# Kernel tuning notes

Measured on AMD Instinct MI355X. Metric: run time of the kernel, lower is better.

The kernel has to match this reference:

```python
import jax, jax.numpy as jnp
import numpy as np

B, IN, H = 8192, 512, 512


def _binarize(w):
    # sign() forward with straight-through gradient (ebnn Binarize)
    return w + jax.lax.stop_gradient(jnp.sign(w) - w)


def setup_inputs() -> dict:
    key = jax.random.key(0)
    ks = jax.random.split(key, 7)
    stdv = 1.0 / np.sqrt(H)
    return {
        "x": jax.random.normal(ks[0], (B, IN), jnp.float32),
        "hx": jax.random.normal(ks[1], (B, H), jnp.float32),
        "cx": jax.random.normal(ks[2], (B, H), jnp.float32),
        "W_ih": jax.random.uniform(ks[3], (4 * H, IN), jnp.float32, -stdv, stdv),
        "W_hh": jax.random.uniform(ks[4], (4 * H, H), jnp.float32, -stdv, stdv),
        "bias_ih": jax.random.uniform(ks[5], (4 * H,), jnp.float32, -stdv, stdv),
        "bias_hh": jax.random.uniform(ks[6], (4 * H,), jnp.float32, -stdv, stdv),
    }


def reference(x, hx, cx, W_ih, W_hh, bias_ih, bias_hh):
    # gates: [B, 4H] = x @ sign(W_ih)^T + b_ih + hx @ sign(W_hh)^T + b_hh
    gates = (jnp.einsum("bi,gi->bg", x, _binarize(W_ih)) + bias_ih
             + jnp.einsum("bh,gh->bg", hx, _binarize(W_hh)) + bias_hh)
    ingate, forgetgate, cellgate, outgate = jnp.split(gates, 4, axis=1)
    cy = jax.nn.sigmoid(forgetgate) * cx + jax.nn.sigmoid(ingate) * jnp.tanh(cellgate)
    hy = jax.nn.sigmoid(outgate) * jnp.tanh(cy)
    return (hy, cy)
```

## Files before the change

kernel.cpp:

```cpp
#include <hip/hip_runtime.h>
#include <hip/hip_bf16.h>
#include <stdint.h>


typedef __attribute__((ext_vector_type(4))) int int4x;
typedef __attribute__((ext_vector_type(4))) float float4x;

#define B_DIM 8192
#define H_DIM 512

__device__ __forceinline__ float bf2f(uint16_t u) {
  return __uint_as_float(((uint32_t)u) << 16);
}
__device__ __forceinline__ uint16_t f2bf(float f) {
  uint32_t u = __float_as_uint(f);
  return (uint16_t)((u + 0x7FFFu + ((u >> 16) & 1u)) >> 16);
}
__device__ __forceinline__ float sigm(float x) { return 1.0f / (1.0f + __expf(-x)); }
__device__ __forceinline__ float tanh_f(float x) { return 2.0f / (1.0f + __expf(-2.0f * x)) - 1.0f; }

__device__ __forceinline__ int detect_f32(const void* x) {
  const int l = threadIdx.x & 63;
  uint32_t wrd = ((const uint32_t*)x)[l];
  uint32_t e0 = (wrd >> 7) & 0xFFu, e1 = (wrd >> 23) & 0xFFu;
  return __ballot(e0 > 0x85u || e1 > 0x85u) != 0ull;
}

__device__ __forceinline__ void quant4(const float* v, uint32_t* hi4, uint32_t* lo4) {
  uint32_t h = 0, lo = 0;
#pragma unroll
  for (int j = 0; j < 4; ++j) {
    float c = fminf(fmaxf(v[j], -8.0f), 8.0f);
    int xf = __float2int_rn(c * 4096.0f);
    xf = xf > 32639 ? 32639 : xf;
    xf = xf < -32768 ? -32768 : xf;
    const int lb = (xf << 24) >> 24;
    const int hb = (xf - lb) >> 8;
    lo |= ((uint32_t)lb & 0xFFu) << (8 * j);
    h |= ((uint32_t)hb & 0xFFu) << (8 * j);
  }
  *hi4 = h;
  *lo4 = lo;
}

__device__ __forceinline__ void gload16(const void* g, void* l) {
  __builtin_amdgcn_global_load_lds(
      (const __attribute__((address_space(1))) unsigned int*)g,
      (__attribute__((address_space(3))) unsigned int*)l, 16, 0, 0);
}

__global__ __launch_bounds__(256) void prep_kernel(
    const void* __restrict__ x, const void* __restrict__ hx,
    const void* __restrict__ w_ih, const void* __restrict__ w_hh,
    int8_t* __restrict__ Xhi, int8_t* __restrict__ Xlo, int8_t* __restrict__ Bp) {
  __shared__ alignas(16) char lsc[33280];
  const int isF32 = detect_f32(x);
  const int t = threadIdx.x;
  const int w = t >> 6, l = t & 63;
  const int isX = blockIdx.x < 512;
  const int grp = isX ? blockIdx.x : (blockIdx.x - 512);

#pragma unroll
  for (int rr = 0; rr < 4; ++rr) {
    const int r = w * 4 + rr;
    long rowbase;
    if (isX) rowbase = (long)(grp * 16 + r) * 512;
    else     rowbase = (long)((grp & 3) * 512 + (grp >> 2) * 16 + r) * 512;
#pragma unroll
    for (int src = 0; src < 2; ++src) {
      const void* sp_ = isX ? (src ? hx : x) : (src ? w_hh : w_ih);
#pragma unroll
      for (int q = 0; q < 2; ++q) {
        const int k = src * 512 + q * 256 + l * 4;
        float v[4];
        if (isF32) {
          float4x f = *(const float4x*)((const float*)sp_ + rowbase + q * 256 + l * 4);
          v[0] = f[0]; v[1] = f[1]; v[2] = f[2]; v[3] = f[3];
        } else {
          const uint16_t* s = (const uint16_t*)sp_ + rowbase + q * 256 + l * 4;
#pragma unroll
          for (int j = 0; j < 4; ++j) v[j] = bf2f(s[j]);
        }
        if (isX) {
          uint32_t h4, lo4;
          quant4(v, &h4, &lo4);
          *(uint32_t*)(lsc + r * 1040 + k) = h4;
          *(uint32_t*)(lsc + 16640 + r * 1040 + k) = lo4;
        } else {
          uint32_t s4 = 0;
#pragma unroll
          for (int j = 0; j < 4; ++j) {
            const int sv = v[j] > 0.f ? 1 : (v[j] < 0.f ? -1 : 0);
            s4 |= ((uint32_t)sv & 0xFFu) << (8 * j);
          }
          *(uint32_t*)(lsc + r * 1040 + k) = s4;
        }
      }
    }
  }
  __syncthreads();
  const int kt = t >> 4, quad = (t >> 2) & 3, rb = (t & 3) * 4;
  const int loff = kt * 64 + quad * 16;
  if (isX) {
    int4x h[4], lo[4];
#pragma unroll
    for (int i = 0; i < 4; ++i) {
      h[i] = *(const int4x*)(lsc + (rb + i) * 1040 + loff);
      lo[i] = *(const int4x*)(lsc + 16640 + (rb + i) * 1040 + loff);
    }
    int4x* dh = (int4x*)(Xhi + (long)grp * 16384 + t * 64);
    int4x* dl = (int4x*)(Xlo + (long)grp * 16384 + t * 64);
#pragma unroll
    for (int i = 0; i < 4; ++i) { dh[i] = h[i]; dl[i] = lo[i]; }
  } else {
    int4x s[4];
#pragma unroll
    for (int i = 0; i < 4; ++i)
      s[i] = *(const int4x*)(lsc + (rb + i) * 1040 + loff);
    int4x* db = (int4x*)(Bp + (long)grp * 16384 + t * 64);
#pragma unroll
    for (int i = 0; i < 4; ++i) db[i] = s[i];
  }
}

__global__ __launch_bounds__(256, 2) void blstm_gemm_kernel(
    const int8_t* __restrict__ Xhi, const int8_t* __restrict__ Xlo,
    const int8_t* __restrict__ Bp, const void* __restrict__ b_ih,
    const void* __restrict__ b_hh, const void* __restrict__ cx,
    const void* __restrict__ xdet, void* __restrict__ out) {
  __shared__ alignas(16) char lds[73728];
  const int tid = threadIdx.x;
  const int l = tid & 63, w = tid >> 6;
  const int lrow = l & 15, lq = l >> 4;
  const int wy = w >> 1, wx = w & 1;
  const int isF32 = detect_f32(xdet);
  const int bid = blockIdx.x;
  const int idx = bid >> 3;
  const int by = (bid & 7) * 8 + (idx >> 4);
  const int bx = idx & 15;

  const int8_t* csrc[6];
  int cdst[6];
#pragma unroll
  for (int i = 0; i < 6; ++i) {
    const int c = w * 6 + i;
    if (c < 8) {
      csrc[i] = Xhi + (((long)(by * 8 + c)) << 14) + l * 16;
      cdst[i] = c * 1024;
    } else if (c < 16) {
      csrc[i] = Xlo + (((long)(by * 8 + (c - 8))) << 14) + l * 16;
      cdst[i] = 8192 + (c - 8) * 1024;
    } else {
      csrc[i] = Bp + (((long)(bx * 8 + (c - 16))) << 14) + l * 16;
      cdst[i] = 16384 + (c - 16) * 1024;
    }
  }

  int4x acch[4][4], accl[4][4];
#pragma unroll
  for (int mt = 0; mt < 4; ++mt)
#pragma unroll
    for (int g = 0; g < 4; ++g) {
      acch[mt][g] = (int4x){0, 0, 0, 0};
      accl[mt][g] = (int4x){0, 0, 0, 0};
    }

#pragma unroll
  for (int i = 0; i < 6; ++i) gload16(csrc[i], lds + cdst[i]);
#pragma unroll
  for (int i = 0; i < 6; ++i) gload16(csrc[i] + 1024, lds + 24576 + cdst[i]);
  asm volatile("s_waitcnt vmcnt(6)\n\ts_barrier" ::: "memory");

#pragma unroll
  for (int ks = 0; ks < 16; ++ks) {
    const int cb = (ks % 3) * 24576;
    if (ks < 14) {
      const int nb = ((ks + 2) % 3) * 24576;
#pragma unroll
      for (int i = 0; i < 6; ++i)
        gload16(csrc[i] + (long)(ks + 2) * 1024, lds + nb + cdst[i]);
    }
    int4x ah[4], al[4], b[4];
#pragma unroll
    for (int mt = 0; mt < 4; ++mt) {
      ah[mt] = *(const int4x*)(lds + cb + (wy * 4 + mt) * 1024 + l * 16);
      al[mt] = *(const int4x*)(lds + cb + 8192 + (wy * 4 + mt) * 1024 + l * 16);
    }
#pragma unroll
    for (int g = 0; g < 4; ++g)
      b[g] = *(const int4x*)(lds + cb + 16384 + (wx * 4 + g) * 1024 + l * 16);
    __builtin_amdgcn_s_setprio(1);
#pragma unroll
    for (int mt = 0; mt < 4; ++mt)
#pragma unroll
      for (int g = 0; g < 4; ++g) {
        acch[mt][g] = __builtin_amdgcn_mfma_i32_16x16x64_i8(ah[mt], b[g], acch[mt][g], 0, 0, 0);
        accl[mt][g] = __builtin_amdgcn_mfma_i32_16x16x64_i8(al[mt], b[g], accl[mt][g], 0, 0, 0);
      }
    __builtin_amdgcn_s_setprio(0);
    if (ks < 14)
      asm volatile("s_waitcnt vmcnt(6)\n\ts_waitcnt lgkmcnt(0)\n\ts_barrier" ::: "memory");
    else if (ks == 14)
      asm volatile("s_waitcnt vmcnt(0)\n\ts_waitcnt lgkmcnt(0)\n\ts_barrier" ::: "memory");
  }

  const long CYo = (long)B_DIM * H_DIM;
  const int c = bx * 32 + wx * 16 + lrow;
  float biasv[4];
#pragma unroll
  for (int g = 0; g < 4; ++g) {
    if (isF32)
      biasv[g] = ((const float*)b_ih)[g * 512 + c] + ((const float*)b_hh)[g * 512 + c];
    else
      biasv[g] = bf2f(((const uint16_t*)b_ih)[g * 512 + c]) + bf2f(((const uint16_t*)b_hh)[g * 512 + c]);
  }
  float* outF = (float*)out;
  uint16_t* outB = (uint16_t*)out;
#pragma unroll
  for (int mt = 0; mt < 4; ++mt) {
#pragma unroll
    for (int r = 0; r < 4; ++r) {
      const int row = by * 128 + wy * 64 + mt * 16 + lq * 4 + r;
      const long cidx = (long)row * H_DIM + c;
      float vg[4];
#pragma unroll
      for (int g = 0; g < 4; ++g)
        vg[g] = fmaf((float)acch[mt][g][r], 0.0625f,
                     fmaf((float)accl[mt][g][r], 2.44140625e-4f, biasv[g]));
      const float cxv = isF32 ? ((const float*)cx)[cidx] : bf2f(((const uint16_t*)cx)[cidx]);
      const float ig = sigm(vg[0]), fg = sigm(vg[1]), og = sigm(vg[3]);
      const float cg = tanh_f(vg[2]);
      const float cy = fg * cxv + ig * cg;
      const float hy = og * tanh_f(cy);
      if (isF32) {
        outF[cidx] = hy;
        outF[CYo + cidx] = cy;
      } else {
        outB[cidx] = f2bf(hy);
        outB[CYo + cidx] = f2bf(cy);
      }
    }
  }
}

extern "C" void kernel_launch(void* const* d_in, const int* in_sizes, int n_in,
                              void* d_out, int out_size, void* d_ws, size_t ws_size,
                              hipStream_t stream) {
  const void* x = d_in[0];
  const void* hx = d_in[1];
  const void* cx = d_in[2];
  const void* W_ih = d_in[3];
  const void* W_hh = d_in[4];
  const void* b_ih = d_in[5];
  const void* b_hh = d_in[6];
  char* ws = (char*)d_ws;
  int8_t* Xhi = (int8_t*)ws;
  int8_t* Xlo = (int8_t*)(ws + 8388608);
  int8_t* Bp = (int8_t*)(ws + 16777216);

  prep_kernel<<<640, 256, 0, stream>>>(x, hx, W_ih, W_hh, Xhi, Xlo, Bp);
  blstm_gemm_kernel<<<1024, 256, 0, stream>>>(Xhi, Xlo, Bp, b_ih, b_hh, cx, x, d_out);
}
```

Baseline: 151.9 us.

## Double-buffer LDS and register fragments to fit three blocks per CU

Shrinks the LDS staging ring from three buffers to two and raises launch bounds to three blocks per CU. It adds a register double-buffer of MFMA operand fragments: the next k-step's fragments are read from LDS while the current step's MFMAs run. The aim is higher occupancy and hiding LDS read latency. In exchange, each step now waits for all global loads to drain (vmcnt(0)) before its barrier, so prefetch distance shrinks, and register pressure rises under a tighter VGPR budget, which risks spills.

```diff
diff --git a/kernel.cpp b/kernel.cpp
--- a/kernel.cpp
+++ b/kernel.cpp
@@ -123,12 +123,12 @@
   }
 }
 
-__global__ __launch_bounds__(256, 2) void blstm_gemm_kernel(
+__global__ __launch_bounds__(256, 3) void blstm_gemm_kernel(
     const int8_t* __restrict__ Xhi, const int8_t* __restrict__ Xlo,
     const int8_t* __restrict__ Bp, const void* __restrict__ b_ih,
     const void* __restrict__ b_hh, const void* __restrict__ cx,
     const void* __restrict__ xdet, void* __restrict__ out) {
-  __shared__ alignas(16) char lds[73728];
+  __shared__ alignas(16) char lds[49152];
   const int tid = threadIdx.x;
   const int l = tid & 63, w = tid >> 6;
   const int lrow = l & 15, lq = l >> 4;
@@ -165,43 +165,55 @@
       accl[mt][g] = (int4x){0, 0, 0, 0};
     }
 
+  int4x fr0[12], fr1[12];
+
 #pragma unroll
   for (int i = 0; i < 6; ++i) gload16(csrc[i], lds + cdst[i]);
 #pragma unroll
   for (int i = 0; i < 6; ++i) gload16(csrc[i] + 1024, lds + 24576 + cdst[i]);
   asm volatile("s_waitcnt vmcnt(6)\n\ts_barrier" ::: "memory");
+#pragma unroll
+  for (int mt = 0; mt < 4; ++mt) {
+    fr0[mt] = *(const int4x*)(lds + (wy * 4 + mt) * 1024 + l * 16);
+    fr0[4 + mt] = *(const int4x*)(lds + 8192 + (wy * 4 + mt) * 1024 + l * 16);
+  }
+#pragma unroll
+  for (int g = 0; g < 4; ++g)
+    fr0[8 + g] = *(const int4x*)(lds + 16384 + (wx * 4 + g) * 1024 + l * 16);
 
 #pragma unroll
   for (int ks = 0; ks < 16; ++ks) {
-    const int cb = (ks % 3) * 24576;
+    const int cur = ks & 1;
+    int4x* const frc = cur ? fr1 : fr0;
+    int4x* const frn = cur ? fr0 : fr1;
+    if (ks < 15) {
+      asm volatile("s_waitcnt vmcnt(0)\n\ts_waitcnt lgkmcnt(0)\n\ts_barrier" ::: "memory");
+    }
     if (ks < 14) {
-      const int nb = ((ks + 2) % 3) * 24576;
 #pragma unroll
       for (int i = 0; i < 6; ++i)
-        gload16(csrc[i] + (long)(ks + 2) * 1024, lds + nb + cdst[i]);
-    }
-    int4x ah[4], al[4], b[4];
-#pragma unroll
-    for (int mt = 0; mt < 4; ++mt) {
-      ah[mt] = *(const int4x*)(lds + cb + (wy * 4 + mt) * 1024 + l * 16);
-      al[mt] = *(const int4x*)(lds + cb + 8192 + (wy * 4 + mt) * 1024 + l * 16);
-    }
-#pragma unroll
-    for (int g = 0; g < 4; ++g)
-      b[g] = *(const int4x*)(lds + cb + 16384 + (wx * 4 + g) * 1024 + l * 16);
+        gload16(csrc[i] + (long)(ks + 2) * 1024, lds + cur * 24576 + cdst[i]);
+    }
+    if (ks < 15) {
+      const int nb = (cur ^ 1) * 24576;
+#pragma unroll
+      for (int mt = 0; mt < 4; ++mt) {
+        frn[mt] = *(const int4x*)(lds + nb + (wy * 4 + mt) * 1024 + l * 16);
+        frn[4 + mt] = *(const int4x*)(lds + nb + 8192 + (wy * 4 + mt) * 1024 + l * 16);
+      }
+#pragma unroll
+      for (int g = 0; g < 4; ++g)
+        frn[8 + g] = *(const int4x*)(lds + nb + 16384 + (wx * 4 + g) * 1024 + l * 16);
+    }
     __builtin_amdgcn_s_setprio(1);
 #pragma unroll
     for (int mt = 0; mt < 4; ++mt)
 #pragma unroll
       for (int g = 0; g < 4; ++g) {
-        acch[mt][g] = __builtin_amdgcn_mfma_i32_16x16x64_i8(ah[mt], b[g], acch[mt][g], 0, 0, 0);
-        accl[mt][g] = __builtin_amdgcn_mfma_i32_16x16x64_i8(al[mt], b[g], accl[mt][g], 0, 0, 0);
+        acch[mt][g] = __builtin_amdgcn_mfma_i32_16x16x64_i8(frc[mt], frc[8 + g], acch[mt][g], 0, 0, 0);
+        accl[mt][g] = __builtin_amdgcn_mfma_i32_16x16x64_i8(frc[4 + mt], frc[8 + g], accl[mt][g], 0, 0, 0);
       }
     __builtin_amdgcn_s_setprio(0);
-    if (ks < 14)
-      asm volatile("s_waitcnt vmcnt(6)\n\ts_waitcnt lgkmcnt(0)\n\ts_barrier" ::: "memory");
-    else if (ks == 14)
-      asm volatile("s_waitcnt vmcnt(0)\n\ts_waitcnt lgkmcnt(0)\n\ts_barrier" ::: "memory");
   }
 
   const long CYo = (long)B_DIM * H_DIM;
```

Result: slower. 523.9 us (+244.8%).

## Double-buffer LDS and register fragments to overlap loads with MFMA

Applied to the files above, without the earlier changes.

Replaces the triple-buffered LDS pipeline with two LDS stages plus register-level double buffering of the A/B fragments. The next stage's fragments are read from LDS into registers before the MFMAs on the current fragments run. Shared memory per block drops from 72KB to 48KB, which may allow more resident blocks. The cost is about 48 extra VGPRs for the second fragment set, and a full vmcnt(0) wait each step that removes the global prefetch depth of two.

```diff
diff --git a/kernel.cpp b/kernel.cpp
--- a/kernel.cpp
+++ b/kernel.cpp
@@ -128,7 +128,7 @@
     const int8_t* __restrict__ Bp, const void* __restrict__ b_ih,
     const void* __restrict__ b_hh, const void* __restrict__ cx,
     const void* __restrict__ xdet, void* __restrict__ out) {
-  __shared__ alignas(16) char lds[73728];
+  __shared__ alignas(16) char lds[49152];
   const int tid = threadIdx.x;
   const int l = tid & 63, w = tid >> 6;
   const int lrow = l & 15, lq = l >> 4;
@@ -165,44 +165,70 @@
       accl[mt][g] = (int4x){0, 0, 0, 0};
     }
 
+  int4x fr0[12], fr1[12];
+
 #pragma unroll
   for (int i = 0; i < 6; ++i) gload16(csrc[i], lds + cdst[i]);
 #pragma unroll
   for (int i = 0; i < 6; ++i) gload16(csrc[i] + 1024, lds + 24576 + cdst[i]);
   asm volatile("s_waitcnt vmcnt(6)\n\ts_barrier" ::: "memory");
-
-#pragma unroll
-  for (int ks = 0; ks < 16; ++ks) {
-    const int cb = (ks % 3) * 24576;
-    if (ks < 14) {
-      const int nb = ((ks + 2) % 3) * 24576;
-#pragma unroll
-      for (int i = 0; i < 6; ++i)
-        gload16(csrc[i] + (long)(ks + 2) * 1024, lds + nb + cdst[i]);
-    }
-    int4x ah[4], al[4], b[4];
-#pragma unroll
-    for (int mt = 0; mt < 4; ++mt) {
-      ah[mt] = *(const int4x*)(lds + cb + (wy * 4 + mt) * 1024 + l * 16);
-      al[mt] = *(const int4x*)(lds + cb + 8192 + (wy * 4 + mt) * 1024 + l * 16);
-    }
-#pragma unroll
-    for (int g = 0; g < 4; ++g)
-      b[g] = *(const int4x*)(lds + cb + 16384 + (wx * 4 + g) * 1024 + l * 16);
-    __builtin_amdgcn_s_setprio(1);
-#pragma unroll
-    for (int mt = 0; mt < 4; ++mt)
-#pragma unroll
-      for (int g = 0; g < 4; ++g) {
-        acch[mt][g] = __builtin_amdgcn_mfma_i32_16x16x64_i8(ah[mt], b[g], acch[mt][g], 0, 0, 0);
-        accl[mt][g] = __builtin_amdgcn_mfma_i32_16x16x64_i8(al[mt], b[g], accl[mt][g], 0, 0, 0);
-      }
-    __builtin_amdgcn_s_setprio(0);
-    if (ks < 14)
-      asm volatile("s_waitcnt vmcnt(6)\n\ts_waitcnt lgkmcnt(0)\n\ts_barrier" ::: "memory");
-    else if (ks == 14)
-      asm volatile("s_waitcnt vmcnt(0)\n\ts_waitcnt lgkmcnt(0)\n\ts_barrier" ::: "memory");
-  }
+#pragma unroll
+  for (int mt = 0; mt < 4; ++mt) {
+    fr0[mt] = *(const int4x*)(lds + (wy * 4 + mt) * 1024 + l * 16);
+    fr0[4 + mt] = *(const int4x*)(lds + 8192 + (wy * 4 + mt) * 1024 + l * 16);
+  }
+#pragma unroll
+  for (int g = 0; g < 4; ++g)
+    fr0[8 + g] = *(const int4x*)(lds + 16384 + (wx * 4 + g) * 1024 + l * 16);
+
+#define STEP(KS, FRC, FRN, CUR)                                                       \
+  do {                                                                                \
+    if ((KS) < 15)                                                                    \
+      asm volatile("s_waitcnt vmcnt(0)\n\ts_waitcnt lgkmcnt(0)\n\ts_barrier" ::: "memory"); \
+    if ((KS) < 14) {                                                                  \
+      _Pragma("unroll")                                                               \
+      for (int i = 0; i < 6; ++i)                                                     \
+        gload16(csrc[i] + (long)((KS) + 2) * 1024, lds + (CUR) * 24576 + cdst[i]);    \
+    }                                                                                 \
+    if ((KS) < 15) {                                                                  \
+      const int nb_ = ((CUR) ^ 1) * 24576;                                            \
+      _Pragma("unroll")                                                               \
+      for (int mt = 0; mt < 4; ++mt) {                                                \
+        FRN[mt] = *(const int4x*)(lds + nb_ + (wy * 4 + mt) * 1024 + l * 16);         \
+        FRN[4 + mt] = *(const int4x*)(lds + nb_ + 8192 + (wy * 4 + mt) * 1024 + l * 16); \
+      }                                                                               \
+      _Pragma("unroll")                                                               \
+      for (int g = 0; g < 4; ++g)                                                     \
+        FRN[8 + g] = *(const int4x*)(lds + nb_ + 16384 + (wx * 4 + g) * 1024 + l * 16); \
+    }                                                                                 \
+    __builtin_amdgcn_s_setprio(1);                                                    \
+    _Pragma("unroll")                                                                 \
+    for (int mt = 0; mt < 4; ++mt)                                                    \
+      _Pragma("unroll")                                                               \
+      for (int g = 0; g < 4; ++g) {                                                   \
+        acch[mt][g] = __builtin_amdgcn_mfma_i32_16x16x64_i8(FRC[mt], FRC[8 + g], acch[mt][g], 0, 0, 0); \
+        accl[mt][g] = __builtin_amdgcn_mfma_i32_16x16x64_i8(FRC[4 + mt], FRC[8 + g], accl[mt][g], 0, 0, 0); \
+      }                                                                               \
+    __builtin_amdgcn_s_setprio(0);                                                    \
+  } while (0)
+
+  STEP(0, fr0, fr1, 0);
+  STEP(1, fr1, fr0, 1);
+  STEP(2, fr0, fr1, 0);
+  STEP(3, fr1, fr0, 1);
+  STEP(4, fr0, fr1, 0);
+  STEP(5, fr1, fr0, 1);
+  STEP(6, fr0, fr1, 0);
+  STEP(7, fr1, fr0, 1);
+  STEP(8, fr0, fr1, 0);
+  STEP(9, fr1, fr0, 1);
+  STEP(10, fr0, fr1, 0);
+  STEP(11, fr1, fr0, 1);
+  STEP(12, fr0, fr1, 0);
+  STEP(13, fr1, fr0, 1);
+  STEP(14, fr0, fr1, 0);
+  STEP(15, fr1, fr0, 1);
+#undef STEP
 
   const long CYo = (long)B_DIM * H_DIM;
   const int c = bx * 32 + wx * 16 + lrow;
```

Result: slower. 165.7 us (+9.1%).
